# Performance work log

Hardware: AMD Instinct MI355X
Metric: run time of the kernel (lower is better)

## Reference

```python
import jax, jax.numpy as jnp
import numpy as np
from jax import lax

# Module config (matches init_kwargs)
C_IN, C_OUT, D_STATE = 512, 256, 16
D_INNER = 2 * C_OUT          # canonical Mamba expand=2
DT_RANK = C_OUT // 16        # ceil(256/16) = 16
D_CONV = 4
BN_EPS = 1e-5


def setup_inputs() -> dict:
    key = jax.random.key(0)
    ks = jax.random.split(key, 16)
    s = 0.02
    B, H, W = 8, 64, 64
    inp = {
        "x": jax.random.normal(ks[0], (B, C_IN, H, W), jnp.float32),
        # lateral 1x1 conv
        "lateral_w": jax.random.normal(ks[1], (C_OUT, C_IN), jnp.float32) * s,
        "lateral_b": jnp.zeros((C_OUT,), jnp.float32),
        # mamba block params
        "in_proj_w": jax.random.normal(ks[2], (2 * D_INNER, C_OUT), jnp.float32) * s,
        "conv1d_w": jax.random.normal(ks[3], (D_INNER, D_CONV), jnp.float32) * s,
        "conv1d_b": jnp.zeros((D_INNER,), jnp.float32),
        "x_proj_w": jax.random.normal(ks[4], (DT_RANK + 2 * D_STATE, D_INNER), jnp.float32) * s,
        "dt_proj_w": jax.random.normal(ks[5], (D_INNER, DT_RANK), jnp.float32) * s,
        "dt_proj_b": jnp.full((D_INNER,), -4.0, jnp.float32),  # softplus -> small dt
        "A_log": jnp.log(jnp.broadcast_to(jnp.arange(1, D_STATE + 1, dtype=jnp.float32), (D_INNER, D_STATE))),  # S4D-real init
        "D_param": jnp.ones((D_INNER,), jnp.float32),
        "out_proj_w": jax.random.normal(ks[6], (C_OUT, D_INNER), jnp.float32) * s,
        # refine: 3x3 conv + BN (eval) + ReLU
        "refine_w": jax.random.normal(ks[7], (C_OUT, C_OUT, 3, 3), jnp.float32) * s,
        "refine_b": jnp.zeros((C_OUT,), jnp.float32),
        "bn_gamma": jnp.ones((C_OUT,), jnp.float32),
        "bn_beta": jnp.zeros((C_OUT,), jnp.float32),
        "bn_mean": jnp.zeros((C_OUT,), jnp.float32),
        "bn_var": jnp.ones((C_OUT,), jnp.float32),
    }
    return inp


def _silu(v):
    return v * jax.nn.sigmoid(v)


def _mamba(u, in_proj_w, conv1d_w, conv1d_b, x_proj_w, dt_proj_w, dt_proj_b,
           A_log, D_param, out_proj_w):
    """Canonical Mamba block on u: (B, L, D) -> (B, L, D)."""
    B, L, D = u.shape
    xz = jnp.einsum('bld,ed->ble', u, in_proj_w)            # (B,L,2*d_inner)
    xm, z = jnp.split(xz, 2, axis=-1)
    # causal depthwise conv1d over L
    xc = xm.transpose(0, 2, 1)                               # (B,d_inner,L)
    xc = lax.conv_general_dilated(xc, conv1d_w[:, None, :], (1,),
                                  [(D_CONV - 1, 0)],
                                  feature_group_count=D_INNER)
    xc = _silu(xc + conv1d_b[None, :, None]).transpose(0, 2, 1)  # (B,L,d_inner)
    proj = jnp.einsum('bld,ed->ble', xc, x_proj_w)           # (B,L,dt_rank+2*N)
    dt_r = proj[..., :DT_RANK]
    B_ssm = proj[..., DT_RANK:DT_RANK + D_STATE]             # (B,L,N)
    C_ssm = proj[..., DT_RANK + D_STATE:]                    # (B,L,N)
    dt = jax.nn.softplus(jnp.einsum('blr,dr->bld', dt_r, dt_proj_w) + dt_proj_b)
    A = -jnp.exp(A_log)                                      # (d_inner,N)

    def step(h, inputs):
        dt_t, B_t, C_t, x_t = inputs                         # (B,d), (B,N), (B,N), (B,d)
        dA = jnp.exp(dt_t[..., None] * A)                    # (B,d,N)
        h = dA * h + dt_t[..., None] * B_t[:, None, :] * x_t[..., None]
        y = jnp.einsum('bdn,bn->bd', h, C_t)
        return h, y

    xs = (dt.transpose(1, 0, 2), B_ssm.transpose(1, 0, 2),
          C_ssm.transpose(1, 0, 2), xc.transpose(1, 0, 2))
    h0 = jnp.zeros((B, D_INNER, D_STATE), u.dtype)
    _, ys = lax.scan(step, h0, xs)                           # (L,B,d_inner)
    y = ys.transpose(1, 0, 2) + xc * D_param
    y = y * _silu(z)
    return jnp.einsum('ble,de->bld', y, out_proj_w)          # (B,L,D)


def reference(x, lateral_w, lateral_b, in_proj_w, conv1d_w, conv1d_b, x_proj_w,
              dt_proj_w, dt_proj_b, A_log, D_param, out_proj_w, refine_w,
              refine_b, bn_gamma, bn_beta, bn_mean, bn_var):
    B, _, H, W = x.shape
    # lateral 1x1 conv
    xl = jnp.einsum('oi,bihw->bohw', lateral_w, x) + lateral_b[None, :, None, None]
    # mamba on flattened spatial sequence, residual add
    u = xl.reshape(B, C_OUT, H * W).transpose(0, 2, 1)        # (B,L,C)
    m = _mamba(u, in_proj_w, conv1d_w, conv1d_b, x_proj_w, dt_proj_w,
               dt_proj_b, A_log, D_param, out_proj_w)
    xr = xl + m.transpose(0, 2, 1).reshape(B, C_OUT, H, W)
    # refine: 3x3 conv + BN(eval) + ReLU
    r = lax.conv_general_dilated(xr, refine_w, (1, 1), [(1, 1), (1, 1)])
    r = r + refine_b[None, :, None, None]
    inv = bn_gamma / jnp.sqrt(bn_var + BN_EPS)
    r = (r - bn_mean[None, :, None, None]) * inv[None, :, None, None] + bn_beta[None, :, None, None]
    return jax.nn.relu(r)
```

## Files before the change

### kernel.cpp

```cpp
#include <hip/hip_runtime.h>
#include <math.h>

#define NB   8
#define CIN  512
#define COUT 256
#define DIN  512
#define LHW  4096
#define NCHK 128
#define CHL  32
#define PW   66
#define PPOS (PW*PW)

typedef __attribute__((ext_vector_type(8))) short bf16x8;
typedef __attribute__((ext_vector_type(4))) float f32x4;

__device__ __forceinline__ float siluf(float v)  { return v / (1.f + __expf(-v)); }
__device__ __forceinline__ float splusf(float v) {
  return fmaxf(v, 0.f) + __logf(1.f + __expf(-fabsf(v)));
}

__device__ __forceinline__ unsigned short f2b(float f) {
  union { float f; unsigned u; } v; v.f = f;
  unsigned r = v.u + 0x7fff + ((v.u >> 16) & 1);
  return (unsigned short)(r >> 16);
}
__device__ __forceinline__ float b2f(unsigned int u) {
  union { unsigned u; float f; } v; v.u = (u & 0xffffu) << 16; return v.f;
}

__device__ __forceinline__ void gload16(const unsigned short* g, unsigned short* l) {
  __builtin_amdgcn_global_load_lds(
      (const __attribute__((address_space(1))) unsigned int*)g,
      (__attribute__((address_space(3))) unsigned int*)l, 16, 0, 0);
}

#define WO1 131072
#define WO2 393216
#define WO3 425984
#define WO4 557056
__global__ __launch_bounds__(256)
void k_wprep(const float* __restrict__ lw, const float* __restrict__ ipw,
             const float* __restrict__ xpw, const float* __restrict__ opw,
             const float* __restrict__ rw, unsigned short* __restrict__ wb) {
  const int i = blockIdx.x * 256 + threadIdx.x;
  if (i < WO1)      wb[i] = f2b(lw[i]);
  else if (i < WO2) wb[i] = f2b(ipw[i - WO1]);
  else if (i < WO3) {
    const int j = i - WO2, row = j >> 9, col = j & 511;
    wb[i] = (row < 48) ? f2b(xpw[row * 512 + col]) : (unsigned short)0;
  }
  else if (i < WO4) wb[i] = f2b(opw[i - WO3]);
  else {
    const int j = i - WO4, o = j / 2304, kk = j % 2304;
    const int tap = kk >> 8, ch = kk & 255;
    wb[i] = f2b(rw[(o * 256 + ch) * 9 + tap]);
  }
}

__global__ __launch_bounds__(256)
void k_wfuse(const float* __restrict__ dtpw, const float* __restrict__ xpw,
             unsigned short* __restrict__ wfb) {
  const int tid = blockIdx.x * 256 + threadIdx.x;
  const int row = tid >> 9, e = tid & 511;
  float v = 0.f;
  if (row < 512) {
#pragma unroll
    for (int r = 0; r < 16; ++r)
      v = fmaf(dtpw[row * 16 + r], xpw[r * 512 + e], v);
  } else if (row < 560) {
    v = xpw[(row - 512) * 512 + e];
  }
  wfb[tid] = f2b(v);
}

__global__ __launch_bounds__(256)
void k_xpose(const float* __restrict__ x, unsigned short* __restrict__ xt) {
  __shared__ unsigned short Ts[64][80];
  const int b  = blockIdx.z;
  const int k0 = blockIdx.y * 64;
  const int l0 = blockIdx.x * 64;
  const int t  = threadIdx.x;
  const int tx = t & 15, ty = t >> 4;
#pragma unroll
  for (int r = 0; r < 4; ++r) {
    const int k = ty + r * 16;
    float4 v = *(const float4*)(x + ((size_t)b * CIN + k0 + k) * LHW + l0 + tx * 4);
    Ts[tx*4+0][k] = f2b(v.x);
    Ts[tx*4+1][k] = f2b(v.y);
    Ts[tx*4+2][k] = f2b(v.z);
    Ts[tx*4+3][k] = f2b(v.w);
  }
  __syncthreads();
  const int lr = t >> 2, kc = (t & 3) * 16;
  unsigned short* dst = xt + ((size_t)b * LHW + l0 + lr) * CIN + k0 + kc;
  *(uint4*)dst       = *(const uint4*)&Ts[lr][kc];
  *(uint4*)(dst + 8) = *(const uint4*)&Ts[lr][kc + 8];
}

template<int RSA, int RSB, int KTOT>
__device__ __forceinline__ void gemm_loop_128(
    const unsigned short* __restrict__ Ab, const unsigned short* __restrict__ Bb,
    unsigned short* As, unsigned short* Bs, int t, f32x4 acc[4][4]) {
  const int w = t >> 6, lane = t & 63;
  const int wm = w >> 1, wn = w & 1;
  const int arow = t >> 2, acol = (t & 3) * 8;
  const int fr = lane & 15, g8 = (lane >> 4) * 8;
  for (int k0 = 0; k0 < KTOT; k0 += 32) {
    __syncthreads();
    gload16(Ab + (size_t)arow * RSA + k0 + acol,        &As[w * 512]);
    gload16(Ab + (size_t)(64 + arow) * RSA + k0 + acol, &As[2048 + w * 512]);
    gload16(Bb + (size_t)arow * RSB + k0 + acol,        &Bs[w * 512]);
    gload16(Bb + (size_t)(64 + arow) * RSB + k0 + acol, &Bs[2048 + w * 512]);
    __syncthreads();
    bf16x8 af[4], bf[4];
#pragma unroll
    for (int f = 0; f < 4; ++f) {
      af[f] = *(const bf16x8*)&As[(wm*64 + f*16 + fr) * 32 + g8];
      bf[f] = *(const bf16x8*)&Bs[(wn*64 + f*16 + fr) * 32 + g8];
    }
#pragma unroll
    for (int i = 0; i < 4; ++i)
#pragma unroll
      for (int j = 0; j < 4; ++j)
        acc[i][j] = __builtin_amdgcn_mfma_f32_16x16x32_bf16(af[i], bf[j], acc[i][j], 0, 0, 0);
  }
}

__global__ __launch_bounds__(256)
void k_lat_mfma(const unsigned short* __restrict__ xt, const unsigned short* __restrict__ lwb,
                const float* __restrict__ lb, unsigned short* __restrict__ ub) {
  __shared__ __align__(16) unsigned short As[4096], Bs[4096];
  const int t = threadIdx.x, lane = t & 63, w = t >> 6;
  const int wm = w >> 1, wn = w & 1;
  const int b = blockIdx.z, m0 = blockIdx.y * 128, n0 = blockIdx.x * 128;
  f32x4 acc[4][4] = {};
  gemm_loop_128<512, 512, 512>(xt + ((size_t)b * LHW + m0) * 512,
                               lwb + (size_t)n0 * 512, As, Bs, t, acc);
  const int fr = lane & 15, q4 = (lane >> 4) * 4;
#pragma unroll
  for (int i = 0; i < 4; ++i) {
    const int l = m0 + wm*64 + i*16 + q4;
#pragma unroll
    for (int j = 0; j < 4; ++j) {
      const int o = n0 + wn*64 + j*16 + fr;
      const float bias = lb[o];
      unsigned short* dst = ub + ((size_t)b * LHW + l) * COUT + o;
#pragma unroll
      for (int q = 0; q < 4; ++q)
        dst[(size_t)q * COUT] = f2b(acc[i][j][q] + bias);
    }
  }
}

__global__ __launch_bounds__(256)
void k_inproj_mfma(const unsigned short* __restrict__ ub, const unsigned short* __restrict__ ipwb,
                   unsigned short* __restrict__ xm_b, unsigned short* __restrict__ zsb) {
  __shared__ __align__(16) unsigned short As[4096], Bs[4096];
  const int t = threadIdx.x, lane = t & 63, w = t >> 6;
  const int wm = w >> 1, wn = w & 1;
  const int b = blockIdx.z, m0 = blockIdx.y * 128, n0 = blockIdx.x * 128;
  f32x4 acc[4][4] = {};
  gemm_loop_128<256, 256, 256>(ub + ((size_t)b * LHW + m0) * 256,
                               ipwb + (size_t)n0 * 256, As, Bs, t, acc);
  const int fr = lane & 15, q4 = (lane >> 4) * 4;
  const bool isz = (n0 >= 512);
#pragma unroll
  for (int i = 0; i < 4; ++i) {
    const int l = m0 + wm*64 + i*16 + q4;
#pragma unroll
    for (int j = 0; j < 4; ++j) {
      const int e = n0 + wn*64 + j*16 + fr;
      if (isz) {
        unsigned short* dst = zsb + ((size_t)b * LHW + l) * DIN + (e - 512);
#pragma unroll
        for (int q = 0; q < 4; ++q)
          dst[(size_t)q * DIN] = f2b(siluf(acc[i][j][q]));
      } else {
        unsigned short* dst = xm_b + ((size_t)b * LHW + l) * DIN + e;
#pragma unroll
        for (int q = 0; q < 4; ++q)
          dst[(size_t)q * DIN] = f2b(acc[i][j][q]);
      }
    }
  }
}

__global__ __launch_bounds__(256)
void k_conv1d(const unsigned short* __restrict__ xm_b, const float* __restrict__ cw,
              const float* __restrict__ cb, unsigned short* __restrict__ xc_b) {
  const int tid = blockIdx.x * 256 + threadIdx.x;
  const int e8 = tid & 63;
  const int lg = tid >> 6;
  const int l0 = (lg & 1023) * 4;
  const int b  = lg >> 10;
  const int e0 = e8 * 8;
  float bias[8];
  *(float4*)&bias[0] = *(const float4*)(cb + e0);
  *(float4*)&bias[4] = *(const float4*)(cb + e0 + 4);
  float wv[8][4];
#pragma unroll
  for (int q = 0; q < 8; ++q) {
    float4 w4 = *(const float4*)(cw + (e0 + q) * 4);
    wv[q][0] = w4.x; wv[q][1] = w4.y; wv[q][2] = w4.z; wv[q][3] = w4.w;
  }
  const unsigned short* base = xm_b + ((size_t)b * LHW + l0) * DIN + e0;
  uint4 rows[7];
  const uint4 z4 = make_uint4(0u, 0u, 0u, 0u);
#pragma unroll
  for (int r = 0; r < 7; ++r) {
    const int ll = r - 3;
    rows[r] = (l0 + ll >= 0) ? *(const uint4*)(base + (ptrdiff_t)ll * DIN) : z4;
  }
  unsigned short* outb = xc_b + ((size_t)b * LHW + l0) * DIN + e0;
#pragma unroll
  for (int j = 0; j < 4; ++j) {
    float acc[8];
#pragma unroll
    for (int q = 0; q < 8; ++q) acc[q] = bias[q];
#pragma unroll
    for (int k = 0; k < 4; ++k) {
      const uint4 raw = rows[j + k];
      acc[0] = fmaf(b2f(raw.x),       wv[0][k], acc[0]);
      acc[1] = fmaf(b2f(raw.x >> 16), wv[1][k], acc[1]);
      acc[2] = fmaf(b2f(raw.y),       wv[2][k], acc[2]);
      acc[3] = fmaf(b2f(raw.y >> 16), wv[3][k], acc[3]);
      acc[4] = fmaf(b2f(raw.z),       wv[4][k], acc[4]);
      acc[5] = fmaf(b2f(raw.z >> 16), wv[5][k], acc[5]);
      acc[6] = fmaf(b2f(raw.w),       wv[6][k], acc[6]);
      acc[7] = fmaf(b2f(raw.w >> 16), wv[7][k], acc[7]);
    }
    uint4 o;
    o.x = (unsigned)f2b(siluf(acc[0])) | ((unsigned)f2b(siluf(acc[1])) << 16);
    o.y = (unsigned)f2b(siluf(acc[2])) | ((unsigned)f2b(siluf(acc[3])) << 16);
    o.z = (unsigned)f2b(siluf(acc[4])) | ((unsigned)f2b(siluf(acc[5])) << 16);
    o.w = (unsigned)f2b(siluf(acc[6])) | ((unsigned)f2b(siluf(acc[7])) << 16);
    *(uint4*)(outb + (size_t)j * DIN) = o;
  }
}

__global__ __launch_bounds__(256)
void k_xdt_mfma(const unsigned short* __restrict__ xc_b, const unsigned short* __restrict__ wfb,
                const float* __restrict__ dtpb,
                unsigned short* __restrict__ dtb, float* __restrict__ proj) {
  __shared__ __align__(16) unsigned short As[4096], Bs[4096];
  const int t = threadIdx.x, lane = t & 63, w = t >> 6;
  const int wm = w >> 1, wn = w & 1;
  const int b = blockIdx.z, m0 = blockIdx.x * 128, n0 = blockIdx.y * 128;
  f32x4 acc[4][4] = {};
  gemm_loop_128<512, 512, 512>(xc_b + ((size_t)b * LHW + m0) * 512,
                               wfb + (size_t)n0 * 512, As, Bs, t, acc);
  const int fr = lane & 15, q4 = (lane >> 4) * 4;
#pragma unroll
  for (int i = 0; i < 4; ++i) {
    const int l = m0 + wm*64 + i*16 + q4;
#pragma unroll
    for (int j = 0; j < 4; ++j) {
      const int c = n0 + wn*64 + j*16 + fr;
      if (c < 512) {
        const float bias = dtpb[c];
        unsigned short* dst = dtb + ((size_t)b * LHW + l) * 512 + c;
#pragma unroll
        for (int q = 0; q < 4; ++q)
          dst[(size_t)q * 512] = f2b(splusf(acc[i][j][q] + bias));
      } else if (c < 560) {
        float* dst = proj + ((size_t)b * LHW + l) * 48 + (c - 512);
#pragma unroll
        for (int q = 0; q < 4; ++q)
          dst[(size_t)q * 48] = acc[i][j][q];
      }
    }
  }
}

__global__ __launch_bounds__(512, 4)
void k_scanA(const float* __restrict__ proj, const unsigned short* __restrict__ dtb,
             const unsigned short* __restrict__ xc_b,
             const float* __restrict__ A_log, float* __restrict__ PS) {
  __shared__ float prs[CHL * 16];
  const int bx = blockIdx.x;
  const int b = bx >> 7, c = bx & 127;
  const int d = threadIdx.x;
  const size_t rbase = (size_t)b * LHW + c * CHL;
  for (int i = d; i < CHL * 4; i += 512) {
    const int row = i >> 2, c4 = i & 3;
    *(float4*)&prs[row * 16 + c4 * 4] = *(const float4*)(proj + (rbase + row) * 48 + 16 + c4 * 4);
  }
  float An[16], h[16];
#pragma unroll
  for (int q = 0; q < 4; ++q) {
    float4 a4 = *(const float4*)(A_log + d*16 + q*4);
    An[q*4+0] = -__expf(a4.x); An[q*4+1] = -__expf(a4.y);
    An[q*4+2] = -__expf(a4.z); An[q*4+3] = -__expf(a4.w);
  }
#pragma unroll
  for (int n = 0; n < 16; ++n) h[n] = 0.f;
  const float An0 = An[0];
  bool lin = true;
#pragma unroll
  for (int n = 1; n < 16; ++n)
    lin = lin && (fabsf(An[n] - (n + 1) * An0) <= 1e-4f * fabsf(An[n]));
  float sdt = 0.f;
  const unsigned short* dt0 = dtb + rbase * 512 + d;
  const unsigned short* xc0 = xc_b + rbase * DIN + d;
  __syncthreads();
  for (int i = 0; i < CHL; ++i) {
    const float dt = b2f(dt0[(size_t)i * 512]);
    sdt += dt;
    const float dtx = dt * b2f(xc0[(size_t)i * DIN]);
    float dA[16];
    if (lin) {
      const float e1 = __expf(dt * An0);
      const float e2 = e1 * e1, e3 = e2 * e1, e4 = e2 * e2;
      dA[0] = e1; dA[1] = e2; dA[2] = e3; dA[3] = e4;
#pragma unroll
      for (int n = 4; n < 16; ++n) dA[n] = dA[n-4] * e4;
    } else {
#pragma unroll
      for (int n = 0; n < 16; ++n) dA[n] = __expf(dt * An[n]);
    }
    const float* pr = &prs[i * 16];
#pragma unroll
    for (int q = 0; q < 4; ++q) {
      float4 B4 = *(const float4*)(pr + q*4);
      h[q*4+0] = fmaf(dA[q*4+0], h[q*4+0], dtx * B4.x);
      h[q*4+1] = fmaf(dA[q*4+1], h[q*4+1], dtx * B4.y);
      h[q*4+2] = fmaf(dA[q*4+2], h[q*4+2], dtx * B4.z);
      h[q*4+3] = fmaf(dA[q*4+3], h[q*4+3], dtx * B4.w);
    }
  }
  float* o = PS + ((size_t)bx * 512 + d) * 32;
#pragma unroll
  for (int q = 0; q < 4; ++q)
    *(float4*)(o + q*4) = make_float4(__expf(sdt*An[q*4+0]), __expf(sdt*An[q*4+1]),
                                      __expf(sdt*An[q*4+2]), __expf(sdt*An[q*4+3]));
#pragma unroll
  for (int q = 0; q < 4; ++q)
    *(float4*)(o + 16 + q*4) = make_float4(h[q*4], h[q*4+1], h[q*4+2], h[q*4+3]);
}

__global__ __launch_bounds__(256)
void k_scanB(const float* __restrict__ PS, float* __restrict__ hst) {
  const int tid = blockIdx.x * 256 + threadIdx.x;
  const int n = tid & 15;
  const int d = (tid >> 4) & 511;
  const int b = tid >> 13;
  float h = 0.f;
  for (int c = 0; c < NCHK; ++c) {
    const size_t idx = (size_t)((b*NCHK + c)*512 + d);
    hst[idx*16 + n] = h;
    h = PS[idx*32 + n] * h + PS[idx*32 + 16 + n];
  }
}

__global__ __launch_bounds__(512, 4)
void k_scanC(const float* __restrict__ proj, const unsigned short* __restrict__ dtb,
             const unsigned short* __restrict__ xc_b,
             const unsigned short* __restrict__ zsb, const float* __restrict__ hst,
             const float* __restrict__ A_log, const float* __restrict__ Dpar,
             unsigned short* __restrict__ ydata) {
  __shared__ float prs[CHL * 32];
  const int bx = blockIdx.x;
  const int b = bx >> 7, c = bx & 127;
  const int d = threadIdx.x;
  const size_t rbase = (size_t)b * LHW + c * CHL;
  for (int i = d; i < CHL * 8; i += 512) {
    const int row = i >> 3, c4 = i & 7;
    *(float4*)&prs[row * 32 + c4 * 4] = *(const float4*)(proj + (rbase + row) * 48 + 16 + c4 * 4);
  }
  float An[16], h[16];
#pragma unroll
  for (int q = 0; q < 4; ++q) {
    float4 a4 = *(const float4*)(A_log + d*16 + q*4);
    An[q*4+0] = -__expf(a4.x); An[q*4+1] = -__expf(a4.y);
    An[q*4+2] = -__expf(a4.z); An[q*4+3] = -__expf(a4.w);
  }
#pragma unroll
  for (int q = 0; q < 4; ++q) {
    float4 h4 = *(const float4*)(hst + ((size_t)bx * 512 + d) * 16 + q*4);
    h[q*4+0] = h4.x; h[q*4+1] = h4.y; h[q*4+2] = h4.z; h[q*4+3] = h4.w;
  }
  const float An0 = An[0];
  bool lin = true;
#pragma unroll
  for (int n = 1; n < 16; ++n)
    lin = lin && (fabsf(An[n] - (n + 1) * An0) <= 1e-4f * fabsf(An[n]));
  const float dp = Dpar[d];
  const unsigned short* dt0 = dtb + rbase * 512 + d;
  const unsigned short* xc0 = xc_b + rbase * DIN + d;
  const unsigned short* zs0 = zsb + rbase * DIN + d;
  unsigned short* y0 = ydata + rbase * DIN + d;
  __syncthreads();
  for (int i = 0; i < CHL; ++i) {
    const float dt = b2f(dt0[(size_t)i * 512]);
    const float xt = b2f(xc0[(size_t)i * DIN]);
    const float zv = b2f(zs0[(size_t)i * DIN]);
    const float dtx = dt * xt;
    float dA[16];
    if (lin) {
      const float e1 = __expf(dt * An0);
      const float e2 = e1 * e1, e3 = e2 * e1, e4 = e2 * e2;
      dA[0] = e1; dA[1] = e2; dA[2] = e3; dA[3] = e4;
#pragma unroll
      for (int n = 4; n < 16; ++n) dA[n] = dA[n-4] * e4;
    } else {
#pragma unroll
      for (int n = 0; n < 16; ++n) dA[n] = __expf(dt * An[n]);
    }
    const float* pr = &prs[i * 32];
    float y0a = 0.f, y1a = 0.f, y2a = 0.f, y3a = 0.f;
#pragma unroll
    for (int q = 0; q < 4; ++q) {
      float4 B4 = *(const float4*)(pr + q*4);
      float4 C4 = *(const float4*)(pr + 16 + q*4);
      h[q*4+0] = fmaf(dA[q*4+0], h[q*4+0], dtx * B4.x);
      h[q*4+1] = fmaf(dA[q*4+1], h[q*4+1], dtx * B4.y);
      h[q*4+2] = fmaf(dA[q*4+2], h[q*4+2], dtx * B4.z);
      h[q*4+3] = fmaf(dA[q*4+3], h[q*4+3], dtx * B4.w);
      y0a = fmaf(h[q*4+0], C4.x, y0a);
      y1a = fmaf(h[q*4+1], C4.y, y1a);
      y2a = fmaf(h[q*4+2], C4.z, y2a);
      y3a = fmaf(h[q*4+3], C4.w, y3a);
    }
    const float y = (y0a + y1a) + (y2a + y3a);
    y0[(size_t)i * DIN] = f2b((y + xt * dp) * zv);
  }
}

__global__ __launch_bounds__(256)
void k_outproj_mfma(const unsigned short* __restrict__ ydata, const unsigned short* __restrict__ opwb,
                    const unsigned short* __restrict__ ub, unsigned short* __restrict__ xrp) {
  __shared__ __align__(16) unsigned short As[4096], Bs[4096];
  const int t = threadIdx.x, lane = t & 63, w = t >> 6;
  const int wm = w >> 1, wn = w & 1;
  const int b = blockIdx.z, m0 = blockIdx.y * 128, n0 = blockIdx.x * 128;
  f32x4 acc[4][4] = {};
  gemm_loop_128<512, 512, 512>(ydata + ((size_t)b * LHW + m0) * 512,
                               opwb + (size_t)n0 * 512, As, Bs, t, acc);
  const int fr = lane & 15, q4 = (lane >> 4) * 4;
#pragma unroll
  for (int i = 0; i < 4; ++i) {
    const int lbase = m0 + wm*64 + i*16 + q4;
#pragma unroll
    for (int q = 0; q < 4; ++q) {
      const int l = lbase + q;
      const int pos = ((l >> 6) + 1) * PW + (l & 63) + 1;
#pragma unroll
      for (int j = 0; j < 4; ++j) {
        const int o = n0 + wn*64 + j*16 + fr;
        const float r = b2f(ub[((size_t)b * LHW + l) * COUT + o]);
        xrp[((size_t)b * PPOS + pos) * COUT + o] = f2b(acc[i][j][q] + r);
      }
    }
  }
}

__global__ __launch_bounds__(256)
void k_refine_mfma(const unsigned short* __restrict__ Aw,
                   const unsigned short* __restrict__ xrp,
                   const float* __restrict__ rb, const float* __restrict__ bng,
                   const float* __restrict__ bnb, const float* __restrict__ bnm,
                   const float* __restrict__ bnv, float* __restrict__ out) {
  __shared__ __align__(16) unsigned short As[4096], Bs[4096];
  const int t = threadIdx.x;
  const int lane = t & 63;
  const int w = t >> 6;
  const int wm = w >> 1, wn = w & 1;
  const int b  = blockIdx.z;
  const int m0 = blockIdx.y * 128;
  const int n0 = blockIdx.x * 128;
  const int y0 = n0 >> 6;
  const unsigned short* xb = xrp + (size_t)b * PPOS * COUT;
  const int arow = t >> 2;
  const int acol = (t & 3) * 8;
  f32x4 acc[4][4] = {};
  for (int ks = 0; ks < 72; ++ks) {
    const int tap = ks >> 3;
    const int i0  = (ks & 7) * 32;
    const int ky  = tap / 3, kx = tap - ky * 3;
    const int k0  = tap * 256 + i0;
    const unsigned short* ga0 = Aw + (size_t)(m0 + arow) * 2304 + k0 + acol;
    const unsigned short* gb0 = xb + ((size_t)((y0 + ky) * PW + kx + arow)) * COUT + i0 + acol;
    __syncthreads();
    gload16(ga0,              &As[w * 512]);
    gload16(ga0 + 64 * 2304,  &As[2048 + w * 512]);
    gload16(gb0,              &Bs[w * 512]);
    gload16(gb0 + PW * COUT,  &Bs[2048 + w * 512]);
    __syncthreads();
    const int fr = lane & 15, g8 = (lane >> 4) * 8;
    bf16x8 af[4], bfr[4];
#pragma unroll
    for (int f = 0; f < 4; ++f) {
      af[f]  = *(const bf16x8*)&As[(wm*64 + f*16 + fr) * 32 + g8];
      bfr[f] = *(const bf16x8*)&Bs[(wn*64 + f*16 + fr) * 32 + g8];
    }
#pragma unroll
    for (int i = 0; i < 4; ++i)
#pragma unroll
      for (int j = 0; j < 4; ++j)
        acc[i][j] = __builtin_amdgcn_mfma_f32_16x16x32_bf16(af[i], bfr[j], acc[i][j], 0, 0, 0);
  }
  const int fr = lane & 15, q4 = (lane >> 4) * 4;
#pragma unroll
  for (int i = 0; i < 4; ++i) {
    const int obase = m0 + wm*64 + i*16 + q4;
#pragma unroll
    for (int q = 0; q < 4; ++q) {
      const int o = obase + q;
      const float inv = bng[o] * rsqrtf(bnv[o] + 1e-5f);
      const float sh  = (rb[o] - bnm[o]) * inv + bnb[o];
      float* orow = out + ((size_t)b * COUT + o) * LHW + n0 + wn*64 + fr;
#pragma unroll
      for (int j = 0; j < 4; ++j)
        orow[j*16] = fmaxf(fmaf(acc[i][j][q], inv, sh), 0.f);
    }
  }
}

extern "C" void kernel_launch(void* const* d_in, const int* in_sizes, int n_in,
                              void* d_out, int out_size, void* d_ws, size_t ws_size,
                              hipStream_t stream) {
  const float* x    = (const float*)d_in[0];
  const float* lw   = (const float*)d_in[1];
  const float* lb   = (const float*)d_in[2];
  const float* ipw  = (const float*)d_in[3];
  const float* cw   = (const float*)d_in[4];
  const float* cb   = (const float*)d_in[5];
  const float* xpw  = (const float*)d_in[6];
  const float* dtpw = (const float*)d_in[7];
  const float* dtpb = (const float*)d_in[8];
  const float* Alog = (const float*)d_in[9];
  const float* Dpar = (const float*)d_in[10];
  const float* opw  = (const float*)d_in[11];
  const float* rw   = (const float*)d_in[12];
  const float* rb   = (const float*)d_in[13];
  const float* bng  = (const float*)d_in[14];
  const float* bnb  = (const float*)d_in[15];
  const float* bnm  = (const float*)d_in[16];
  const float* bnv  = (const float*)d_in[17];
  float* out = (float*)d_out;

  float* ws = (float*)d_ws;
  unsigned short* ub   = (unsigned short*)ws;
  unsigned short* xt   = (unsigned short*)(ws + 4194304);
  unsigned short* xm_b = (unsigned short*)(ws + 12582912);
  unsigned short* xc_b = (unsigned short*)(ws + 20971520);
  unsigned short* zsb  = (unsigned short*)(ws + 29360128);
  float* proj = ws + 37748736;
  float* PS   = ws + 39321600;
  float* hst  = ws + 56098816;
  unsigned short* wb  = (unsigned short*)(ws + 64487424);
  unsigned short* wfb = (unsigned short*)(ws + 65060864);
  unsigned short* lwb  = wb;
  unsigned short* ipwb = wb + WO1;
  unsigned short* opwb = wb + WO3;
  unsigned short* Aw   = wb + WO4;
  unsigned short* ydata = xm_b;
  unsigned short* dtb   = xt;
  unsigned short* xrp   = xt;

  k_wprep<<<dim3(4480), 256, 0, stream>>>(lw, ipw, xpw, opw, rw, wb);
  k_wfuse<<<dim3(1280), 256, 0, stream>>>(dtpw, xpw, wfb);
  k_xpose<<<dim3(64, 8, 8), 256, 0, stream>>>(x, xt);
  k_lat_mfma<<<dim3(2, 32, 8), 256, 0, stream>>>(xt, lwb, lb, ub);
  k_inproj_mfma<<<dim3(8, 32, 8), 256, 0, stream>>>(ub, ipwb, xm_b, zsb);
  k_conv1d<<<dim3(2048), 256, 0, stream>>>(xm_b, cw, cb, xc_b);
  k_xdt_mfma<<<dim3(32, 5, 8), 256, 0, stream>>>(xc_b, wfb, dtpb, dtb, proj);
  k_scanA<<<dim3(NB * NCHK), 512, 0, stream>>>(proj, dtb, xc_b, Alog, PS);
  k_scanB<<<dim3(256), 256, 0, stream>>>(PS, hst);
  k_scanC<<<dim3(NB * NCHK), 512, 0, stream>>>(proj, dtb, xc_b, zsb, hst, Alog, Dpar, ydata);
  hipMemsetAsync(xrp, 0, (size_t)NB * PPOS * COUT * sizeof(unsigned short), stream);
  k_outproj_mfma<<<dim3(2, 32, 8), 256, 0, stream>>>(ydata, opwb, ub, xrp);
  k_refine_mfma<<<dim3(32, 2, 8), 256, 0, stream>>>(Aw, xrp, rb, bng, bnb, bnm, bnv, out);
}
```

Baseline: 372.3 us.

## Double-buffer LDS tiles and XOR-swizzle layout in MFMA GEMM and refine loops

The shared GEMM k-loop and the 3x3 refine conv loop now use two LDS buffers. The next K-slice is issued into one buffer while MFMAs consume the other, which removes one of the two barriers per iteration. Tile columns are also XOR-swizzled on the row index for both the global-to-LDS stores and the fragment reads, to cut LDS bank conflicts. LDS use per block doubles to 32 KB, which may lower occupancy.

After: 378.7 us. No clear change (+1.7%).

```diff
diff --git a/kernel.cpp b/kernel.cpp
--- a/kernel.cpp
+++ b/kernel.cpp
@@ -100,36 +100,47 @@
 template<int RSA, int RSB, int KTOT>
 __device__ __forceinline__ void gemm_loop_128(
     const unsigned short* __restrict__ Ab, const unsigned short* __restrict__ Bb,
-    unsigned short* As, unsigned short* Bs, int t, f32x4 acc[4][4]) {
+    unsigned short (&As)[2][4096], unsigned short (&Bs)[2][4096],
+    int t, f32x4 acc[4][4]) {
   const int w = t >> 6, lane = t & 63;
   const int wm = w >> 1, wn = w & 1;
-  const int arow = t >> 2, acol = (t & 3) * 8;
-  const int fr = lane & 15, g8 = (lane >> 4) * 8;
+  const int arow = t >> 2;
+  const int acol = (((t & 3) ^ ((t >> 3) & 3))) * 8;
+  const int fr = lane & 15;
+  const int g8 = (((lane >> 4)) * 8) ^ (((fr >> 1) & 3) * 8);
+
+#define GL128_STAGE(k0, buf)                                                     \
+  gload16(Ab + (size_t)arow * RSA + (k0) + acol,        &As[buf][w * 512]);      \
+  gload16(Ab + (size_t)(64 + arow) * RSA + (k0) + acol, &As[buf][2048 + w*512]); \
+  gload16(Bb + (size_t)arow * RSB + (k0) + acol,        &Bs[buf][w * 512]);      \
+  gload16(Bb + (size_t)(64 + arow) * RSB + (k0) + acol, &Bs[buf][2048 + w*512]);
+
+  GL128_STAGE(0, 0);
+  __syncthreads();
+  int cur = 0;
   for (int k0 = 0; k0 < KTOT; k0 += 32) {
-    __syncthreads();
-    gload16(Ab + (size_t)arow * RSA + k0 + acol,        &As[w * 512]);
-    gload16(Ab + (size_t)(64 + arow) * RSA + k0 + acol, &As[2048 + w * 512]);
-    gload16(Bb + (size_t)arow * RSB + k0 + acol,        &Bs[w * 512]);
-    gload16(Bb + (size_t)(64 + arow) * RSB + k0 + acol, &Bs[2048 + w * 512]);
-    __syncthreads();
+    if (k0 + 32 < KTOT) { GL128_STAGE(k0 + 32, cur ^ 1); }
     bf16x8 af[4], bf[4];
 #pragma unroll
     for (int f = 0; f < 4; ++f) {
-      af[f] = *(const bf16x8*)&As[(wm*64 + f*16 + fr) * 32 + g8];
-      bf[f] = *(const bf16x8*)&Bs[(wn*64 + f*16 + fr) * 32 + g8];
+      af[f] = *(const bf16x8*)&As[cur][(wm*64 + f*16 + fr) * 32 + g8];
+      bf[f] = *(const bf16x8*)&Bs[cur][(wn*64 + f*16 + fr) * 32 + g8];
     }
 #pragma unroll
     for (int i = 0; i < 4; ++i)
 #pragma unroll
       for (int j = 0; j < 4; ++j)
         acc[i][j] = __builtin_amdgcn_mfma_f32_16x16x32_bf16(af[i], bf[j], acc[i][j], 0, 0, 0);
-  }
+    __syncthreads();
+    cur ^= 1;
+  }
+#undef GL128_STAGE
 }
 
 __global__ __launch_bounds__(256)
 void k_lat_mfma(const unsigned short* __restrict__ xt, const unsigned short* __restrict__ lwb,
                 const float* __restrict__ lb, unsigned short* __restrict__ ub) {
-  __shared__ __align__(16) unsigned short As[4096], Bs[4096];
+  __shared__ __align__(16) unsigned short As[2][4096], Bs[2][4096];
   const int t = threadIdx.x, lane = t & 63, w = t >> 6;
   const int wm = w >> 1, wn = w & 1;
   const int b = blockIdx.z, m0 = blockIdx.y * 128, n0 = blockIdx.x * 128;
@@ -155,7 +166,7 @@
 __global__ __launch_bounds__(256)
 void k_inproj_mfma(const unsigned short* __restrict__ ub, const unsigned short* __restrict__ ipwb,
                    unsigned short* __restrict__ xm_b, unsigned short* __restrict__ zsb) {
-  __shared__ __align__(16) unsigned short As[4096], Bs[4096];
+  __shared__ __align__(16) unsigned short As[2][4096], Bs[2][4096];
   const int t = threadIdx.x, lane = t & 63, w = t >> 6;
   const int wm = w >> 1, wn = w & 1;
   const int b = blockIdx.z, m0 = blockIdx.y * 128, n0 = blockIdx.x * 128;
@@ -242,7 +253,7 @@
 void k_xdt_mfma(const unsigned short* __restrict__ xc_b, const unsigned short* __restrict__ wfb,
                 const float* __restrict__ dtpb,
                 unsigned short* __restrict__ dtb, float* __restrict__ proj) {
-  __shared__ __align__(16) unsigned short As[4096], Bs[4096];
+  __shared__ __align__(16) unsigned short As[2][4096], Bs[2][4096];
   const int t = threadIdx.x, lane = t & 63, w = t >> 6;
   const int wm = w >> 1, wn = w & 1;
   const int b = blockIdx.z, m0 = blockIdx.x * 128, n0 = blockIdx.y * 128;
@@ -429,7 +440,7 @@
 __global__ __launch_bounds__(256)
 void k_outproj_mfma(const unsigned short* __restrict__ ydata, const unsigned short* __restrict__ opwb,
                     const unsigned short* __restrict__ ub, unsigned short* __restrict__ xrp) {
-  __shared__ __align__(16) unsigned short As[4096], Bs[4096];
+  __shared__ __align__(16) unsigned short As[2][4096], Bs[2][4096];
   const int t = threadIdx.x, lane = t & 63, w = t >> 6;
   const int wm = w >> 1, wn = w & 1;
   const int b = blockIdx.z, m0 = blockIdx.y * 128, n0 = blockIdx.x * 128;
@@ -460,7 +471,7 @@
                    const float* __restrict__ rb, const float* __restrict__ bng,
                    const float* __restrict__ bnb, const float* __restrict__ bnm,
                    const float* __restrict__ bnv, float* __restrict__ out) {
-  __shared__ __align__(16) unsigned short As[4096], Bs[4096];
+  __shared__ __align__(16) unsigned short As[2][4096], Bs[2][4096];
   const int t = threadIdx.x;
   const int lane = t & 63;
   const int w = t >> 6;
@@ -471,35 +482,45 @@
   const int y0 = n0 >> 6;
   const unsigned short* xb = xrp + (size_t)b * PPOS * COUT;
   const int arow = t >> 2;
-  const int acol = (t & 3) * 8;
+  const int acol = (((t & 3) ^ ((t >> 3) & 3))) * 8;
+  const int fr = lane & 15;
+  const int g8 = (((lane >> 4)) * 8) ^ (((fr >> 1) & 3) * 8);
+
+#define RF_STAGE(ks, buf) {                                                            \
+    const int tap_ = (ks) >> 3;                                                        \
+    const int i0_  = ((ks) & 7) * 32;                                                  \
+    const int ky_  = tap_ / 3, kx_ = tap_ - ky_ * 3;                                   \
+    const int k0_  = tap_ * 256 + i0_;                                                 \
+    const unsigned short* ga_ = Aw + (size_t)(m0 + arow) * 2304 + k0_ + acol;          \
+    const unsigned short* gb_ = xb + ((size_t)((y0 + ky_) * PW + kx_ + arow)) * COUT + i0_ + acol; \
+    gload16(ga_,              &As[buf][w * 512]);                                      \
+    gload16(ga_ + 64 * 2304,  &As[buf][2048 + w * 512]);                               \
+    gload16(gb_,              &Bs[buf][w * 512]);                                      \
+    gload16(gb_ + PW * COUT,  &Bs[buf][2048 + w * 512]);                               \
+  }
+
   f32x4 acc[4][4] = {};
+  RF_STAGE(0, 0);
+  __syncthreads();
+  int cur = 0;
   for (int ks = 0; ks < 72; ++ks) {
-    const int tap = ks >> 3;
-    const int i0  = (ks & 7) * 32;
-    const int ky  = tap / 3, kx = tap - ky * 3;
-    const int k0  = tap * 256 + i0;
-    const unsigned short* ga0 = Aw + (size_t)(m0 + arow) * 2304 + k0 + acol;
-    const unsigned short* gb0 = xb + ((size_t)((y0 + ky) * PW + kx + arow)) * COUT + i0 + acol;
-    __syncthreads();
-    gload16(ga0,              &As[w * 512]);
-    gload16(ga0 + 64 * 2304,  &As[2048 + w * 512]);
-    gload16(gb0,              &Bs[w * 512]);
-    gload16(gb0 + PW * COUT,  &Bs[2048 + w * 512]);
-    __syncthreads();
-    const int fr = lane & 15, g8 = (lane >> 4) * 8;
+    if (ks + 1 < 72) RF_STAGE(ks + 1, cur ^ 1);
     bf16x8 af[4], bfr[4];
 #pragma unroll
     for (int f = 0; f < 4; ++f) {
-      af[f]  = *(const bf16x8*)&As[(wm*64 + f*16 + fr) * 32 + g8];
-      bfr[f] = *(const bf16x8*)&Bs[(wn*64 + f*16 + fr) * 32 + g8];
+      af[f]  = *(const bf16x8*)&As[cur][(wm*64 + f*16 + fr) * 32 + g8];
+      bfr[f] = *(const bf16x8*)&Bs[cur][(wn*64 + f*16 + fr) * 32 + g8];
     }
 #pragma unroll
     for (int i = 0; i < 4; ++i)
 #pragma unroll
       for (int j = 0; j < 4; ++j)
         acc[i][j] = __builtin_amdgcn_mfma_f32_16x16x32_bf16(af[i], bfr[j], acc[i][j], 0, 0, 0);
-  }
-  const int fr = lane & 15, q4 = (lane >> 4) * 4;
+    __syncthreads();
+    cur ^= 1;
+  }
+#undef RF_STAGE
+  const int q4 = (lane >> 4) * 4;
 #pragma unroll
   for (int i = 0; i < 4; ++i) {
     const int obase = m0 + wm*64 + i*16 + q4;
```
